# Kernel optimization log

Hardware: AMD Instinct MI355X
Metric: run time of the kernel (lower is better)

Reference implementation:

```python
import jax, jax.numpy as jnp
import numpy as np

HIDDEN = 2048
N_HEADS = 16
HEAD_DIM = HIDDEN // N_HEADS
MAX_POS = 4096
ROPE_THETA = 10000.0
B, S = 2, 4096


def rotate_half(x):
    d = x.shape[-1] // 2
    return jnp.concatenate([-x[..., d:], x[..., :d]], axis=-1)


def make_rope_cache(seq_len, dim, base):
    inv_freq = 1.0 / (base ** (np.arange(0, dim, 2, dtype=np.float32) / dim))
    t = np.arange(seq_len, dtype=np.float32)
    freqs = np.einsum('i,j->ij', t, inv_freq)
    emb = np.concatenate([freqs, freqs], axis=-1)
    return jnp.asarray(np.cos(emb)), jnp.asarray(np.sin(emb))


def setup_inputs() -> dict:
    key = jax.random.key(0)
    k1, k2, k3, k4, k5, k6 = jax.random.split(key, 6)
    hidden_states = jax.random.normal(k1, (B, S, HIDDEN), dtype=jnp.float32)
    # causal additive mask [B,1,S,S]
    causal = jnp.where(jnp.tril(jnp.ones((S, S), dtype=bool)), 0.0, -1e9).astype(jnp.float32)
    attention_mask = jnp.broadcast_to(causal[None, None], (B, 1, S, S))
    position_ids = jnp.broadcast_to(jnp.arange(S, dtype=jnp.int64)[None], (B, S))
    scale = 0.02
    Wq = jax.random.normal(k2, (HIDDEN, HIDDEN), dtype=jnp.float32) * scale
    Wk = jax.random.normal(k3, (HIDDEN, HIDDEN), dtype=jnp.float32) * scale
    Wv = jax.random.normal(k4, (HIDDEN, HIDDEN), dtype=jnp.float32) * scale
    Wo = jax.random.normal(k5, (HIDDEN, HIDDEN), dtype=jnp.float32) * scale
    return {"hidden_states": hidden_states, "attention_mask": attention_mask,
            "position_ids": position_ids, "Wq": Wq, "Wk": Wk, "Wv": Wv, "Wo": Wo}


def reference(hidden_states, attention_mask, position_ids, Wq, Wk, Wv, Wo):
    bsz, q_len, _ = hidden_states.shape
    # projections (torch Linear: x @ W.T; here W stored as [in,out] -> x @ W)
    q = (hidden_states @ Wq).reshape(bsz, q_len, N_HEADS, HEAD_DIM).transpose(0, 2, 1, 3)
    k = (hidden_states @ Wk).reshape(bsz, q_len, N_HEADS, HEAD_DIM).transpose(0, 2, 1, 3)
    v = (hidden_states @ Wv).reshape(bsz, q_len, N_HEADS, HEAD_DIM).transpose(0, 2, 1, 3)
    cos_c, sin_c = make_rope_cache(q_len, HEAD_DIM, ROPE_THETA)
    cos = cos_c[position_ids][:, None]  # [B,1,S,Dh]
    sin = sin_c[position_ids][:, None]
    q = q * cos + rotate_half(q) * sin
    k = k * cos + rotate_half(k) * sin
    scores = jnp.einsum('bhqd,bhkd->bhqk', q, k) / jnp.sqrt(jnp.float32(HEAD_DIM))
    scores = scores + attention_mask
    probs = jax.nn.softmax(scores.astype(jnp.float32), axis=-1).astype(q.dtype)
    attn = jnp.einsum('bhqk,bhkd->bhqd', probs, v)
    attn = attn.transpose(0, 2, 1, 3).reshape(bsz, q_len, HIDDEN)
    return attn @ Wo
```

## Files before the change

kernel.cpp:

```cpp
#include <hip/hip_runtime.h>

#define HID 2048
#define NHEADS 16
#define DHEAD 128
#define BB 2
#define SS 4096
#define MTOT (BB * SS)

typedef __attribute__((ext_vector_type(8))) short short8;
typedef __attribute__((ext_vector_type(8))) unsigned short ushort8;
typedef __attribute__((ext_vector_type(4))) float floatx4;
typedef __attribute__((ext_vector_type(16))) float floatx16;

static __device__ __forceinline__ ushort f2bf(float f) {
  unsigned x = __float_as_uint(f);
  return (ushort)((x + 0x7fffu + ((x >> 16) & 1u)) >> 16);
}
static __device__ __forceinline__ float bf2f(ushort u) {
  return __uint_as_float(((unsigned)u) << 16);
}
static __device__ __forceinline__ unsigned cvtpk_bf16(float lo, float hi) {
  unsigned r;
  asm("v_cvt_pk_bf16_f32 %0, %1, %2" : "=v"(r) : "v"(lo), "v"(hi));
  return r;
}
static __device__ __forceinline__ void pl32swap(unsigned& a, unsigned& b) {
  asm volatile("v_permlane32_swap_b32 %0, %1" : "+v"(a), "+v"(b));
}
static __device__ __forceinline__ floatx16 fz16() {
  floatx16 z;
#pragma unroll
  for (int i = 0; i < 16; i++) z[i] = 0.f;
  return z;
}

#define GL16(g, l)                                                   \
  __builtin_amdgcn_global_load_lds(                                  \
      (const __attribute__((address_space(1))) unsigned int*)(g),    \
      (__attribute__((address_space(3))) unsigned int*)(l), 16, 0, 0)

__global__ void k_cvt_bf16(const float* __restrict__ x, ushort* __restrict__ o, int n4) {
  int i = blockIdx.x * blockDim.x + threadIdx.x;
  int stride = gridDim.x * blockDim.x;
  for (; i < n4; i += stride) {
    float4 v = reinterpret_cast<const float4*>(x)[i];
    ushort4 u;
    u.x = f2bf(v.x); u.y = f2bf(v.y); u.z = f2bf(v.z); u.w = f2bf(v.w);
    reinterpret_cast<ushort4*>(o)[i] = u;
  }
}

__global__ __launch_bounds__(256) void k_wt(const float* __restrict__ W, ushort* __restrict__ Wt) {
  __shared__ float tile[64][65];
  int n0 = blockIdx.x * 64, k0 = blockIdx.y * 64;
  int t = threadIdx.x;
#pragma unroll
  for (int i = 0; i < 16; i++) {
    int idx = t + i * 256, r = idx >> 6, c = idx & 63;
    tile[r][c] = W[(size_t)(k0 + r) * HID + n0 + c];
  }
  __syncthreads();
#pragma unroll
  for (int i = 0; i < 16; i++) {
    int idx = t + i * 256, r = idx >> 6, c = idx & 63;
    Wt[(size_t)(n0 + r) * HID + k0 + c] = f2bf(tile[c][r]);
  }
}

__global__ void k_rope_tab(float* __restrict__ cosT, float* __restrict__ sinT) {
  int idx = blockIdx.x * 256 + threadIdx.x;
  int pos = idx >> 6, j = idx & 63;
  float inv = powf(10000.0f, -(float)(2 * j) * (1.0f / 128.0f));
  float a = (float)pos * inv;
  cosT[idx] = cosf(a);
  sinT[idx] = sinf(a);
}

__global__ void k_rope(ushort* __restrict__ Q, ushort* __restrict__ Kb,
                       const float* __restrict__ cosT, const float* __restrict__ sinT) {
  const float kSc = 0.12751742f;
  int idx = blockIdx.x * 256 + threadIdx.x;
  int j8 = (idx & 7) * 8;
  int hh = (idx >> 3) & (NHEADS - 1);
  int srow = idx >> 7;
  int pos = srow & (SS - 1);
  float4 c0 = *reinterpret_cast<const float4*>(&cosT[pos * 64 + j8]);
  float4 c1 = *reinterpret_cast<const float4*>(&cosT[pos * 64 + j8 + 4]);
  float4 s0 = *reinterpret_cast<const float4*>(&sinT[pos * 64 + j8]);
  float4 s1 = *reinterpret_cast<const float4*>(&sinT[pos * 64 + j8 + 4]);
  float cc[8] = {c0.x, c0.y, c0.z, c0.w, c1.x, c1.y, c1.z, c1.w};
  float ss[8] = {s0.x, s0.y, s0.z, s0.w, s1.x, s1.y, s1.z, s1.w};
  size_t base = (size_t)srow * HID + hh * DHEAD + j8;
  ushort8 qa = *reinterpret_cast<ushort8*>(&Q[base]);
  ushort8 qb = *reinterpret_cast<ushort8*>(&Q[base + 64]);
  ushort8 ka = *reinterpret_cast<ushort8*>(&Kb[base]);
  ushort8 kb = *reinterpret_cast<ushort8*>(&Kb[base + 64]);
  ushort8 o1, o2, o3, o4;
#pragma unroll
  for (int i = 0; i < 8; i++) {
    float a1 = bf2f(qa[i]), a2 = bf2f(qb[i]);
    o1[i] = f2bf((a1 * cc[i] - a2 * ss[i]) * kSc);
    o2[i] = f2bf((a2 * cc[i] + a1 * ss[i]) * kSc);
    float b1 = bf2f(ka[i]), b2 = bf2f(kb[i]);
    o3[i] = f2bf(b1 * cc[i] - b2 * ss[i]);
    o4[i] = f2bf(b2 * cc[i] + b1 * ss[i]);
  }
  *reinterpret_cast<ushort8*>(&Q[base]) = o1;
  *reinterpret_cast<ushort8*>(&Q[base + 64]) = o2;
  *reinterpret_cast<ushort8*>(&Kb[base]) = o3;
  *reinterpret_cast<ushort8*>(&Kb[base + 64]) = o4;
}

template <int OUT_BF16>
__global__ __launch_bounds__(512, 2) void k_gemm8(const ushort* __restrict__ A,
                                                  const ushort* __restrict__ Bt,
                                                  void* __restrict__ Cp,
                                                  int Mr, int Nc, int Kd) {
  __shared__ ushort As[3][256 * 32];
  __shared__ ushort Bs[3][256 * 32];
  int t = threadIdx.x;
  int lane = t & 63, wid = t >> 6;
  int lrow = lane & 15, lk = lane >> 4;
  int wr = wid >> 2, wc = wid & 3;

  int nbx = Nc >> 8;
  int cpx = gridDim.x >> 3;
  int id = blockIdx.x;
  int swz = (id & 7) * cpx + (id >> 3);
  int m0 = (swz / nbx) << 8, n0 = (swz % nbx) << 8;

  floatx4 acc[8][4];
#pragma unroll
  for (int i = 0; i < 8; i++)
#pragma unroll
    for (int j = 0; j < 4; j++) acc[i][j] = (floatx4){0.f, 0.f, 0.f, 0.f};

  int arow = t >> 2;
  int acol = (((t & 3) ^ (arow & 3)) << 3);
  const ushort* gA = A + (size_t)(m0 + arow) * Kd + acol;
  const ushort* gB = Bt + (size_t)(n0 + arow) * Kd + acol;

  auto STAGE = [&](int buf, int kt) {
    const ushort* a = gA + kt * 32;
    const ushort* bq = gB + kt * 32;
    GL16(a, (char*)As + buf * 16384 + t * 16);
    GL16(a + (size_t)128 * Kd, (char*)As + buf * 16384 + t * 16 + 8192);
    GL16(bq, (char*)Bs + buf * 16384 + t * 16);
    GL16(bq + (size_t)128 * Kd, (char*)Bs + buf * 16384 + t * 16 + 8192);
  };

  STAGE(0, 0);
  STAGE(1, 1);

  int nk = Kd >> 5;
  for (int tK = 0; tK < nk; ++tK) {
    if (tK + 1 < nk)
      asm volatile("s_waitcnt vmcnt(4)" ::: "memory");
    else
      asm volatile("s_waitcnt vmcnt(0)" ::: "memory");
    __builtin_amdgcn_s_barrier();
    asm volatile("" ::: "memory");
    int buf = tK % 3;
    const char* Ab_ = (const char*)As + buf * 16384;
    const char* Bb_ = (const char*)Bs + buf * 16384;
    short8 af[8], bfr[4];
#pragma unroll
    for (int fm = 0; fm < 8; fm++) {
      int row = wr * 128 + fm * 16 + lrow;
      af[fm] = *reinterpret_cast<const short8*>(
          Ab_ + ((row * 64 + lk * 16) ^ ((row & 3) << 4)));
    }
#pragma unroll
    for (int fn = 0; fn < 4; fn++) {
      int row = wc * 64 + fn * 16 + lrow;
      bfr[fn] = *reinterpret_cast<const short8*>(
          Bb_ + ((row * 64 + lk * 16) ^ ((row & 3) << 4)));
    }
    if (tK + 2 < nk) STAGE((tK + 2) % 3, tK + 2);
    __builtin_amdgcn_s_setprio(1);
#pragma unroll
    for (int fm = 0; fm < 8; fm++)
#pragma unroll
      for (int fn = 0; fn < 4; fn++)
        acc[fm][fn] = __builtin_amdgcn_mfma_f32_16x16x32_bf16(af[fm], bfr[fn],
                                                              acc[fm][fn], 0, 0, 0);
    __builtin_amdgcn_s_setprio(0);
  }

#pragma unroll
  for (int am = 0; am < 8; am++)
#pragma unroll
    for (int an = 0; an < 4; an++)
#pragma unroll
      for (int r = 0; r < 4; r++) {
        int m = m0 + wr * 128 + am * 16 + lk * 4 + r;
        int n = n0 + wc * 64 + an * 16 + lrow;
        if (OUT_BF16)
          ((ushort*)Cp)[(size_t)m * Nc + n] = f2bf(acc[am][an][r]);
        else
          ((float*)Cp)[(size_t)m * Nc + n] = acc[am][an][r];
      }
}

__global__ __launch_bounds__(256, 2) void k_fattn(const ushort* __restrict__ Qg,
                                                  const ushort* __restrict__ Kg,
                                                  const ushort* __restrict__ Vt2,
                                                  ushort* __restrict__ Og) {
  __shared__ ushort Ks[2][64 * 128];
  __shared__ ushort Vs[2][128 * 64];
  int t = threadIdx.x, lane = t & 63, wid = t >> 6;
  int l31 = lane & 31, hi = lane >> 5;
  int id = blockIdx.x;
  int xcd = id & 7, slot = id >> 3;
  int pi = slot & 15;
  int grp = xcd + 8 * (slot >> 4);
  int h = grp & 15, b = grp >> 4;

  auto STAGE = [&](int buf, int kt) {
    int kv0 = kt * 64;
    const ushort* Kbase = Kg + (size_t)(b * SS + kv0) * HID + h * DHEAD;
    const ushort* Vbase = Vt2 + (size_t)(h * DHEAD) * MTOT + b * SS + kv0;
#pragma unroll
    for (int i = 0; i < 4; i++) {
      int L = t + i * 256;
      int row = L >> 4, cr = L & 15;
      GL16(Kbase + (size_t)row * HID + ((cr ^ (row & 15)) << 3),
           (char*)Ks + buf * 16384 + L * 16);
    }
#pragma unroll
    for (int i = 0; i < 4; i++) {
      int L = t + i * 256;
      int row = L >> 3, cr = L & 7;
      GL16(Vbase + (size_t)row * MTOT + ((cr ^ (row & 7)) << 3),
           (char*)Vs + buf * 16384 + L * 16);
    }
  };

  for (int e = 0; e < 2; e++) {
    int qt = e ? (31 - pi) : pi;
    int q0 = qt * 128;
    int wq0 = q0 + wid * 32;
    int qlane = wq0 + l31;

    short8 qf[8];
    {
      const ushort* qb = Qg + (size_t)(b * SS + qlane) * HID + h * DHEAD + hi * 8;
#pragma unroll
      for (int ks = 0; ks < 8; ks++)
        qf[ks] = *reinterpret_cast<const short8*>(qb + ks * 16);
    }

    floatx16 accO[4];
#pragma unroll
    for (int db = 0; db < 4; db++) accO[db] = fz16();
    float mrow = -1e30f, lsum = 0.f;

    int nkt = (qt + 1) * 2;
    STAGE(0, 0);
    __syncthreads();

    for (int kt = 0; kt < nkt; kt++) {
      int cur = kt & 1;
      int kv0 = kt * 64;
      if (kt + 1 < nkt) STAGE(cur ^ 1, kt + 1);

      if (kv0 <= wq0 + 31) {
        const char* Kb_ = (const char*)Ks + cur * 16384;
        floatx16 accS[2];
        accS[0] = fz16(); accS[1] = fz16();
        __builtin_amdgcn_s_setprio(1);
#pragma unroll
        for (int ks = 0; ks < 8; ks++) {
#pragma unroll
          for (int kvb = 0; kvb < 2; kvb++) {
            int row = kvb * 32 + l31;
            int byte_ = (row * 256 + ks * 32 + hi * 16) ^ ((row & 15) << 4);
            short8 kf = *reinterpret_cast<const short8*>(Kb_ + byte_);
            accS[kvb] = __builtin_amdgcn_mfma_f32_32x32x16_bf16(kf, qf[ks], accS[kvb], 0, 0, 0);
          }
        }
        __builtin_amdgcn_s_setprio(0);

        if (kv0 + 63 > wq0) {
          int kvbase = kv0 + hi * 4;
#pragma unroll
          for (int kvb = 0; kvb < 2; kvb++)
#pragma unroll
            for (int r = 0; r < 16; r++) {
              int kvi = kvbase + kvb * 32 + (r & 3) + 8 * (r >> 2);
              if (kvi > qlane) accS[kvb][r] = -1e30f;
            }
        }

        float mA = -1e30f, mB = -1e30f, mC = -1e30f, mD = -1e30f;
#pragma unroll
        for (int r = 0; r < 16; r += 4) {
          mA = fmaxf(mA, fmaxf(accS[0][r], accS[1][r]));
          mB = fmaxf(mB, fmaxf(accS[0][r + 1], accS[1][r + 1]));
          mC = fmaxf(mC, fmaxf(accS[0][r + 2], accS[1][r + 2]));
          mD = fmaxf(mD, fmaxf(accS[0][r + 3], accS[1][r + 3]));
        }
        float mx = fmaxf(fmaxf(mA, mB), fmaxf(mC, mD));
        mx = fmaxf(mx, __shfl_xor(mx, 32));
        if (!__all(mx <= mrow + 8.0f)) {
          float mnew = fmaxf(mrow, mx);
          float corr = exp2f(mrow - mnew);
          mrow = mnew;
          lsum *= corr;
#pragma unroll
          for (int db = 0; db < 4; db++)
#pragma unroll
            for (int r = 0; r < 16; r++) accO[db][r] *= corr;
        }

        float sA = 0.f, sB = 0.f, sC = 0.f, sD = 0.f;
#pragma unroll
        for (int kvb = 0; kvb < 2; kvb++)
#pragma unroll
          for (int r = 0; r < 16; r += 4) {
            float p0 = exp2f(accS[kvb][r] - mrow);
            float p1 = exp2f(accS[kvb][r + 1] - mrow);
            float p2 = exp2f(accS[kvb][r + 2] - mrow);
            float p3 = exp2f(accS[kvb][r + 3] - mrow);
            accS[kvb][r] = p0; accS[kvb][r + 1] = p1;
            accS[kvb][r + 2] = p2; accS[kvb][r + 3] = p3;
            sA += p0; sB += p1; sC += p2; sD += p3;
          }
        lsum += ((sA + sB) + (sC + sD));

        const char* Vb_ = (const char*)Vs + cur * 16384;
#pragma unroll
        for (int ks = 0; ks < 4; ks++) {
          int kvb = ks >> 1, tt = ks & 1;
          unsigned w0 = cvtpk_bf16(accS[kvb][8 * tt + 0], accS[kvb][8 * tt + 1]);
          unsigned w2 = cvtpk_bf16(accS[kvb][8 * tt + 4], accS[kvb][8 * tt + 5]);
          pl32swap(w0, w2);
          unsigned w1 = cvtpk_bf16(accS[kvb][8 * tt + 2], accS[kvb][8 * tt + 3]);
          unsigned w3 = cvtpk_bf16(accS[kvb][8 * tt + 6], accS[kvb][8 * tt + 7]);
          pl32swap(w1, w3);
          union { unsigned u[4]; short8 v; } pf;
          pf.u[0] = w0; pf.u[1] = w1; pf.u[2] = w2; pf.u[3] = w3;
          __builtin_amdgcn_s_setprio(1);
#pragma unroll
          for (int db = 0; db < 4; db++) {
            int row = db * 32 + l31;
            int byte_ = (row * 128 + ks * 32 + hi * 16) ^ ((row & 7) << 4);
            short8 vf = *reinterpret_cast<const short8*>(Vb_ + byte_);
            accO[db] = __builtin_amdgcn_mfma_f32_32x32x16_bf16(vf, pf.v, accO[db], 0, 0, 0);
          }
          __builtin_amdgcn_s_setprio(0);
        }
      }
      __syncthreads();
    }

    float lt = lsum + __shfl_xor(lsum, 32);
    float inv = 1.0f / lt;
    char* sb = (char*)Ks + wid * 8192;
#pragma unroll
    for (int db = 0; db < 4; db++)
#pragma unroll
      for (int r = 0; r < 16; r += 2) {
        int d = db * 32 + (r & 3) + 8 * (r >> 2) + hi * 4;
        unsigned w = cvtpk_bf16(accO[db][r] * inv, accO[db][r + 1] * inv);
        int byte_ = (l31 * 256 + d * 2) ^ ((l31 & 15) << 4);
        *reinterpret_cast<unsigned*>(sb + byte_) = w;
      }
#pragma unroll
    for (int i = 0; i < 8; i++) {
      int row = i * 4 + (lane >> 4);
      int byte_ = (row * 256 + (lane & 15) * 16) ^ ((row & 15) << 4);
      ushort8 ov = *reinterpret_cast<const ushort8*>(sb + byte_);
      *reinterpret_cast<ushort8*>(Og + (size_t)(b * SS + wq0 + row) * HID + h * DHEAD +
                                  (lane & 15) * 8) = ov;
    }
    __syncthreads();
  }
}

extern "C" void kernel_launch(void* const* d_in, const int* in_sizes, int n_in,
                              void* d_out, int out_size, void* d_ws, size_t ws_size,
                              hipStream_t stream) {
  const float* X = (const float*)d_in[0];
  const float* Wq = (const float*)d_in[3];
  const float* Wk = (const float*)d_in[4];
  const float* Wv = (const float*)d_in[5];
  const float* Wo = (const float*)d_in[6];
  float* out = (float*)d_out;

  char* p = (char*)d_ws;
  const size_t szXb = (size_t)MTOT * HID * 2;
  const size_t szW = (size_t)HID * HID * 2;
  ushort* Xb = (ushort*)p;  p += szXb;
  ushort* Wqt = (ushort*)p; p += szW;
  ushort* Wkt = (ushort*)p; p += szW;
  ushort* Wvt = (ushort*)p; p += szW;
  ushort* Wot = (ushort*)p; p += szW;
  ushort* Qb = (ushort*)p;  p += szXb;
  ushort* Kb = (ushort*)p;  p += szXb;
  ushort* Vt2 = (ushort*)p; p += szXb;
  ushort* Ab = (ushort*)p;  p += szXb;
  float* cosT = (float*)p;  p += (size_t)SS * 64 * 4;
  float* sinT = (float*)p;  p += (size_t)SS * 64 * 4;

  k_cvt_bf16<<<2048, 256, 0, stream>>>(X, Xb, MTOT * HID / 4);
  dim3 wg(32, 32);
  k_wt<<<wg, 256, 0, stream>>>(Wq, Wqt);
  k_wt<<<wg, 256, 0, stream>>>(Wk, Wkt);
  k_wt<<<wg, 256, 0, stream>>>(Wv, Wvt);
  k_wt<<<wg, 256, 0, stream>>>(Wo, Wot);
  k_rope_tab<<<SS * 64 / 256, 256, 0, stream>>>(cosT, sinT);

  int gqk = (MTOT / 256) * (HID / 256);
  k_gemm8<1><<<gqk, 512, 0, stream>>>(Xb, Wqt, Qb, MTOT, HID, HID);
  k_gemm8<1><<<gqk, 512, 0, stream>>>(Xb, Wkt, Kb, MTOT, HID, HID);
  int gv = (HID / 256) * (MTOT / 256);
  k_gemm8<1><<<gv, 512, 0, stream>>>(Wvt, Xb, Vt2, HID, MTOT, HID);

  k_rope<<<MTOT * NHEADS * 8 / 256, 256, 0, stream>>>(Qb, Kb, cosT, sinT);

  k_fattn<<<512, 256, 0, stream>>>(Qb, Kb, Vt2, Ab);

  k_gemm8<0><<<gqk, 512, 0, stream>>>(Ab, Wot, out, MTOT, HID, HID);
}
```

Baseline: 570.9 us.

## Merge prep kernels into one launch, fuse Q/K GEMMs, simplify attention grid

The input conversion, four weight transposes and the RoPE table build are folded into a single k_prep launch dispatched by block-id range. The Q and K projections run as one 512-block dual GEMM that switches its B matrix and output pointer by block id, so the two GEMMs fill the device together. The attention kernel drops its XCD-aware block remapping in favour of a plain 3D grid, which may change L2 locality across XCDs. The intent is to cut launch gaps and tail underutilisation across the small kernels.

```diff
diff --git a/kernel.cpp b/kernel.cpp
--- a/kernel.cpp
+++ b/kernel.cpp
@@ -39,41 +39,54 @@
       (const __attribute__((address_space(1))) unsigned int*)(g),    \
       (__attribute__((address_space(3))) unsigned int*)(l), 16, 0, 0)
 
-__global__ void k_cvt_bf16(const float* __restrict__ x, ushort* __restrict__ o, int n4) {
-  int i = blockIdx.x * blockDim.x + threadIdx.x;
-  int stride = gridDim.x * blockDim.x;
-  for (; i < n4; i += stride) {
-    float4 v = reinterpret_cast<const float4*>(x)[i];
-    ushort4 u;
-    u.x = f2bf(v.x); u.y = f2bf(v.y); u.z = f2bf(v.z); u.w = f2bf(v.w);
-    reinterpret_cast<ushort4*>(o)[i] = u;
+__global__ __launch_bounds__(256) void k_prep(const float* __restrict__ X,
+                                              ushort* __restrict__ Xb,
+                                              const float* __restrict__ Wq,
+                                              const float* __restrict__ Wk,
+                                              const float* __restrict__ Wv,
+                                              const float* __restrict__ Wo,
+                                              ushort* __restrict__ Wqt,
+                                              ushort* __restrict__ Wkt,
+                                              ushort* __restrict__ Wvt,
+                                              ushort* __restrict__ Wot,
+                                              float* __restrict__ cosT,
+                                              float* __restrict__ sinT) {
+  __shared__ float tile[64][65];
+  int id = blockIdx.x, t = threadIdx.x;
+  if (id < 2048) {
+    int i = id * 256 + t;
+    const int n4 = MTOT * HID / 4, stride = 2048 * 256;
+    for (; i < n4; i += stride) {
+      float4 v = reinterpret_cast<const float4*>(X)[i];
+      ushort4 u;
+      u.x = f2bf(v.x); u.y = f2bf(v.y); u.z = f2bf(v.z); u.w = f2bf(v.w);
+      reinterpret_cast<ushort4*>(Xb)[i] = u;
+    }
+  } else if (id < 6144) {
+    int w = (id - 2048) >> 10;
+    int bid = (id - 2048) & 1023;
+    const float* W = (w == 0) ? Wq : (w == 1) ? Wk : (w == 2) ? Wv : Wo;
+    ushort* Wt = (w == 0) ? Wqt : (w == 1) ? Wkt : (w == 2) ? Wvt : Wot;
+    int n0 = (bid & 31) * 64, k0 = (bid >> 5) * 64;
+#pragma unroll
+    for (int i = 0; i < 16; i++) {
+      int idx = t + i * 256, r = idx >> 6, c = idx & 63;
+      tile[r][c] = W[(size_t)(k0 + r) * HID + n0 + c];
+    }
+    __syncthreads();
+#pragma unroll
+    for (int i = 0; i < 16; i++) {
+      int idx = t + i * 256, r = idx >> 6, c = idx & 63;
+      Wt[(size_t)(n0 + r) * HID + k0 + c] = f2bf(tile[c][r]);
+    }
+  } else {
+    int idx = (id - 6144) * 256 + t;
+    int pos = idx >> 6, j = idx & 63;
+    float inv = powf(10000.0f, -(float)(2 * j) * (1.0f / 128.0f));
+    float a = (float)pos * inv;
+    cosT[idx] = cosf(a);
+    sinT[idx] = sinf(a);
   }
-}
-
-__global__ __launch_bounds__(256) void k_wt(const float* __restrict__ W, ushort* __restrict__ Wt) {
-  __shared__ float tile[64][65];
-  int n0 = blockIdx.x * 64, k0 = blockIdx.y * 64;
-  int t = threadIdx.x;
-#pragma unroll
-  for (int i = 0; i < 16; i++) {
-    int idx = t + i * 256, r = idx >> 6, c = idx & 63;
-    tile[r][c] = W[(size_t)(k0 + r) * HID + n0 + c];
-  }
-  __syncthreads();
-#pragma unroll
-  for (int i = 0; i < 16; i++) {
-    int idx = t + i * 256, r = idx >> 6, c = idx & 63;
-    Wt[(size_t)(n0 + r) * HID + k0 + c] = f2bf(tile[c][r]);
-  }
-}
-
-__global__ void k_rope_tab(float* __restrict__ cosT, float* __restrict__ sinT) {
-  int idx = blockIdx.x * 256 + threadIdx.x;
-  int pos = idx >> 6, j = idx & 63;
-  float inv = powf(10000.0f, -(float)(2 * j) * (1.0f / 128.0f));
-  float a = (float)pos * inv;
-  cosT[idx] = cosf(a);
-  sinT[idx] = sinf(a);
 }
 
 __global__ void k_rope(ushort* __restrict__ Q, ushort* __restrict__ Kb,
@@ -111,10 +124,12 @@
   *reinterpret_cast<ushort8*>(&Kb[base + 64]) = o4;
 }
 
-template <int OUT_BF16>
+template <int OUT_BF16, int DUAL>
 __global__ __launch_bounds__(512, 2) void k_gemm8(const ushort* __restrict__ A,
                                                   const ushort* __restrict__ Bt,
                                                   void* __restrict__ Cp,
+                                                  const ushort* __restrict__ Bt2,
+                                                  void* __restrict__ Cp2,
                                                   int Mr, int Nc, int Kd) {
   __shared__ ushort As[3][256 * 32];
   __shared__ ushort Bs[3][256 * 32];
@@ -123,10 +138,14 @@
   int lrow = lane & 15, lk = lane >> 4;
   int wr = wid >> 2, wc = wid & 3;
 
+  int id = blockIdx.x;
+  if (DUAL && id >= 256) {
+    Bt = Bt2;
+    Cp = Cp2;
+    id -= 256;
+  }
   int nbx = Nc >> 8;
-  int cpx = gridDim.x >> 3;
-  int id = blockIdx.x;
-  int swz = (id & 7) * cpx + (id >> 3);
+  int swz = (id & 7) * 32 + (id >> 3);
   int m0 = (swz / nbx) << 8, n0 = (swz % nbx) << 8;
 
   floatx4 acc[8][4];
@@ -210,11 +229,7 @@
   __shared__ ushort Vs[2][128 * 64];
   int t = threadIdx.x, lane = t & 63, wid = t >> 6;
   int l31 = lane & 31, hi = lane >> 5;
-  int id = blockIdx.x;
-  int xcd = id & 7, slot = id >> 3;
-  int pi = slot & 15;
-  int grp = xcd + 8 * (slot >> 4);
-  int h = grp & 15, b = grp >> 4;
+  int pi = blockIdx.x, h = blockIdx.y, b = blockIdx.z;
 
   auto STAGE = [&](int buf, int kt) {
     int kv0 = kt * 64;
@@ -403,23 +418,16 @@
   float* cosT = (float*)p;  p += (size_t)SS * 64 * 4;
   float* sinT = (float*)p;  p += (size_t)SS * 64 * 4;
 
-  k_cvt_bf16<<<2048, 256, 0, stream>>>(X, Xb, MTOT * HID / 4);
-  dim3 wg(32, 32);
-  k_wt<<<wg, 256, 0, stream>>>(Wq, Wqt);
-  k_wt<<<wg, 256, 0, stream>>>(Wk, Wkt);
-  k_wt<<<wg, 256, 0, stream>>>(Wv, Wvt);
-  k_wt<<<wg, 256, 0, stream>>>(Wo, Wot);
-  k_rope_tab<<<SS * 64 / 256, 256, 0, stream>>>(cosT, sinT);
-
-  int gqk = (MTOT / 256) * (HID / 256);
-  k_gemm8<1><<<gqk, 512, 0, stream>>>(Xb, Wqt, Qb, MTOT, HID, HID);
-  k_gemm8<1><<<gqk, 512, 0, stream>>>(Xb, Wkt, Kb, MTOT, HID, HID);
-  int gv = (HID / 256) * (MTOT / 256);
-  k_gemm8<1><<<gv, 512, 0, stream>>>(Wvt, Xb, Vt2, HID, MTOT, HID);
+  k_prep<<<7168, 256, 0, stream>>>(X, Xb, Wq, Wk, Wv, Wo, Wqt, Wkt, Wvt, Wot,
+                                   cosT, sinT);
+
+  k_gemm8<1, 1><<<512, 512, 0, stream>>>(Xb, Wqt, Qb, Wkt, Kb, MTOT, HID, HID);
+  k_gemm8<1, 0><<<256, 512, 0, stream>>>(Wvt, Xb, Vt2, nullptr, nullptr, HID, MTOT, HID);
 
   k_rope<<<MTOT * NHEADS * 8 / 256, 256, 0, stream>>>(Qb, Kb, cosT, sinT);
 
-  k_fattn<<<512, 256, 0, stream>>>(Qb, Kb, Vt2, Ab);
-
-  k_gemm8<0><<<gqk, 512, 0, stream>>>(Ab, Wot, out, MTOT, HID, HID);
-}
+  dim3 ag(16, NHEADS, BB);
+  k_fattn<<<ag, 256, 0, stream>>>(Qb, Kb, Vt2, Ab);
+
+  k_gemm8<0, 0><<<256, 512, 0, stream>>>(Ab, Wot, out, nullptr, nullptr, MTOT, HID, HID);
+}
```

New measurement: 541.4 us. -5.2%, faster.
